# Optimization experiments

Measured on AMD Instinct MI355X. Metric: run time of the kernel, lower is better.

Reference implementation:

```python
import jax, jax.numpy as jnp
import numpy as np

N, E = 100000, 1600000          # nodes, edges
DIN, DH, DOUT = 128, 128, 64    # input_dim, hidden_dim, output_dim


def setup_inputs() -> dict:
    key = jax.random.key(0)
    k0, k1, k2, k3 = jax.random.split(key, 4)
    x = jax.random.normal(k0, (N, DIN), dtype=jnp.float32)
    edge_index = jax.random.randint(k1, (2, E), 0, N)
    # GCNConv params (glorot-ish weights, zero bias)
    W1 = jax.random.normal(k2, (DIN, DH), dtype=jnp.float32) / np.sqrt(DIN).astype(np.float32)
    b1 = jnp.zeros((DH,), jnp.float32)
    W2 = jax.random.normal(k3, (DH, DOUT), dtype=jnp.float32) / np.sqrt(DH).astype(np.float32)
    b2 = jnp.zeros((DOUT,), jnp.float32)
    return {"x": x, "edge_index": edge_index, "W1": W1, "b1": b1, "W2": W2, "b2": b2}


def _gcn_conv(h_in, W, b, src, dst, norm_e, self_norm, n):
    # PyG GCNConv: transform, then normalized sum-aggregation with self-loops.
    h = h_in @ W                                   # [N, dout]
    msg = h[src] * norm_e[:, None]                 # [E, dout] gather + edge scale
    agg = jax.ops.segment_sum(msg, dst, num_segments=n)
    agg = agg + h * self_norm[:, None]             # self-loop contribution (norm = 1/deg)
    return agg + b


def reference(x, edge_index, W1, b1, W2, b2):
    src, dst = edge_index[0], edge_index[1]
    n = x.shape[0]
    # degree including self-loop, computed on dst (PyG convention)
    deg = jax.ops.segment_sum(jnp.ones((src.shape[0],), x.dtype), dst, num_segments=n) + 1.0
    dinv = jax.lax.rsqrt(deg)
    norm_e = dinv[src] * dinv[dst]                 # per-edge D^-1/2 A D^-1/2
    self_norm = dinv * dinv
    h = _gcn_conv(x, W1, b1, src, dst, norm_e, self_norm, n)
    h = jax.nn.relu(h)                             # dropout is identity in eval mode
    out = _gcn_conv(h, W2, b2, src, dst, norm_e, self_norm, n)
    return out
```

## Files before the change

kernel.cpp:

```cpp
#include <hip/hip_runtime.h>

#define NN 100000
#define NE 1600000
#define NBUCK 1563
#define NBH 256
#define CHUNK 6250
#define NSEG 8
#define SEGC (NBH/NSEG)
#define NBXB 12500
#define NBG 1563
#define NBGG 782


typedef short bf16x8 __attribute__((ext_vector_type(8)));
typedef float f32x4  __attribute__((ext_vector_type(4)));
typedef float f32x2  __attribute__((ext_vector_type(2)));

__device__ __forceinline__ float b2f(unsigned short u) {
    return __uint_as_float(((unsigned int)u) << 16);
}
__device__ __forceinline__ unsigned short f2b(float f) {
    unsigned int x = __float_as_uint(f);
    x += 0x7FFFu + ((x >> 16) & 1u);
    return (unsigned short)(x >> 16);
}

__global__ __launch_bounds__(256) void k_pre(const float* __restrict__ x,
                                             unsigned short* __restrict__ xb,
                                             const int* __restrict__ dst,
                                             int* __restrict__ ghist,
                                             const float* __restrict__ W1,
                                             const float* __restrict__ W2,
                                             unsigned short* __restrict__ Wg1,
                                             unsigned short* __restrict__ Wg2) {
    int b = blockIdx.x;
    if (b < NBXB) {
        int id = b * 256 + threadIdx.x;
        float4 v = ((const float4*)x)[id];
        ushort4 o;
        o.x = f2b(v.x); o.y = f2b(v.y); o.z = f2b(v.z); o.w = f2b(v.w);
        ((ushort4*)xb)[id] = o;
        return;
    }
    if (b == NBXB + NBH) {
        for (int i = threadIdx.x; i < 16384; i += 256) {
            int j = i & 7, l = (i >> 3) & 63, ks = (i >> 9) & 3, ct = i >> 11;
            int k = ks * 32 + ((l >> 4) << 3) + j;
            int c = ct * 16 + (l & 15);
            Wg1[i] = f2b(W1[k * 128 + c]);
        }
        return;
    }
    if (b == NBXB + NBH + 1) {
        for (int i = threadIdx.x; i < 8192; i += 256) {
            int j = i & 7, l = (i >> 3) & 63, ks = (i >> 9) & 3, ct = i >> 11;
            int k = ks * 32 + ((l >> 4) << 3) + j;
            int c = ct * 16 + (l & 15);
            Wg2[i] = f2b(W2[k * 64 + c]);
        }
        return;
    }
    __shared__ int h[NBUCK];
    int tid = threadIdx.x;
    int i = b - NBXB;
    for (int k = tid; k < NBUCK; k += 256) h[k] = 0;
    __syncthreads();
    int e0 = i * CHUNK;
    for (int e = e0 + tid; e < e0 + CHUNK; e += 256) {
        unsigned d = (unsigned)dst[e];
        if (d < NN) atomicAdd(&h[d >> 6], 1);
    }
    __syncthreads();
    for (int k = tid; k < NBUCK; k += 256) ghist[i * NBUCK + k] = h[k];
}

__global__ __launch_bounds__(256) void k_scanB(const int* __restrict__ ghist,
                                               int* __restrict__ boffT,
                                               int* __restrict__ tot) {
    __shared__ int part[NSEG][32];
    int kk = threadIdx.x & 31, seg = threadIdx.x >> 5;
    int k = blockIdx.x * 32 + kk;
    bool ok = (k < NBUCK);
    int i0 = seg * SEGC;
    int S = 0;
    if (ok) {
#pragma unroll 8
        for (int i = i0; i < i0 + SEGC; ++i) S += ghist[i * NBUCK + k];
    }
    part[seg][kk] = S;
    __syncthreads();
    int pre = 0;
#pragma unroll
    for (int s2 = 0; s2 < NSEG; ++s2) pre += (s2 < seg) ? part[s2][kk] : 0;
    if (ok) {
        int run = pre;
#pragma unroll 8
        for (int i = i0; i < i0 + SEGC; ++i) {
            int c = ghist[i * NBUCK + k];
            boffT[i * NBUCK + k] = run;
            run += c;
        }
        if (seg == NSEG - 1) tot[k] = run;
    }
}

__global__ __launch_bounds__(256) void k_place(const int* __restrict__ src,
                                               const int* __restrict__ dst,
                                               const int* __restrict__ tot,
                                               const int* __restrict__ boffT,
                                               int* __restrict__ ebuf,
                                               int* __restrict__ bbase_out) {
    __shared__ int cur[NBUCK];
    __shared__ int s[256];
    const int tid = threadIdx.x, bid = blockIdx.x;
    const int i = ((bid & 7) * (NBH / 8)) + (bid >> 3);
    int k0 = tid * 7;
    int v[7]; int S = 0;
#pragma unroll
    for (int q = 0; q < 7; ++q) {
        int k = k0 + q;
        v[q] = (k < NBUCK) ? tot[k] : 0;
        S += v[q];
    }
    s[tid] = S;
    __syncthreads();
    for (int off = 1; off < 256; off <<= 1) {
        int t = (tid >= off) ? s[tid - off] : 0;
        __syncthreads();
        s[tid] += t;
        __syncthreads();
    }
    int run = s[tid] - S;
#pragma unroll
    for (int q = 0; q < 7; ++q) {
        int k = k0 + q;
        if (k < NBUCK) {
            cur[k] = run + boffT[i * NBUCK + k];
            if (bid == 0) bbase_out[k] = run;
            run += v[q];
        }
    }
    __syncthreads();
    int e0 = i * CHUNK;
    for (int e = e0 + tid; e < e0 + CHUNK; e += 256) {
        unsigned d = (unsigned)dst[e];
        if (d >= NN) continue;
        unsigned sv = (unsigned)src[e];
        if (sv >= NN) sv = 0;
        int pos = atomicAdd(&cur[d >> 6], 1);
        ebuf[pos] = (int)(sv | ((d & 63u) << 17));
    }
}

__global__ __launch_bounds__(256) void k_binC(const int* __restrict__ bbase,
                                              const int* __restrict__ tot,
                                              const int* __restrict__ ebuf,
                                              int* __restrict__ row_start,
                                              float* __restrict__ dinv,
                                              int* __restrict__ csr) {
    __shared__ int cnt[64], excl[64], cur[64];
    int b = blockIdx.x, tid = threadIdx.x;
    int n0 = b * 64;
    int base = bbase[b], end = base + tot[b];
    if (tid < 64) cnt[tid] = 0;
    __syncthreads();
    for (int i = base + tid; i < end; i += 256)
        atomicAdd(&cnt[((unsigned)ebuf[i]) >> 17], 1);
    __syncthreads();
    if (tid == 0) {
        int run = 0;
        for (int t = 0; t < 64; ++t) { excl[t] = run; run += cnt[t]; }
    }
    __syncthreads();
    if (tid < 64) {
        int node = n0 + tid;
        if (node < NN) {
            row_start[node] = base + excl[tid];
            dinv[node] = rsqrtf((float)cnt[tid] + 1.0f);
        }
        cur[tid] = base + excl[tid];
    }
    if (b == NBUCK - 1 && tid == 0) row_start[NN] = end;
    __syncthreads();
    for (int i = base + tid; i < end; i += 256) {
        unsigned rec = (unsigned)ebuf[i];
        int pos = atomicAdd(&cur[rec >> 17], 1);
        csr[pos] = (int)(rec & 0x1FFFFu);
    }
}

__global__ __launch_bounds__(256) void k_agg1(const unsigned short* __restrict__ xb,
                                              const float* __restrict__ dinv,
                                              const int* __restrict__ row_start,
                                              const int* __restrict__ csr,
                                              char* __restrict__ P) {
    int node = blockIdx.x * 4 + (threadIdx.x >> 6);
    int lane = threadIdx.x & 63;
    int sub  = lane >> 4;
    int dimb = lane & 15;
    const uint4* X4 = (const uint4*)xb;
    float dv = dinv[node];
    float sn4 = dv * dv * 0.25f;
    uint4 sv = X4[(size_t)node * 16 + dimb];
    f32x2 a0, a1, a2, a3;
    a0.x = __uint_as_float(sv.x << 16) * sn4;  a0.y = __uint_as_float(sv.x & 0xFFFF0000u) * sn4;
    a1.x = __uint_as_float(sv.y << 16) * sn4;  a1.y = __uint_as_float(sv.y & 0xFFFF0000u) * sn4;
    a2.x = __uint_as_float(sv.z << 16) * sn4;  a2.y = __uint_as_float(sv.z & 0xFFFF0000u) * sn4;
    a3.x = __uint_as_float(sv.w << 16) * sn4;  a3.y = __uint_as_float(sv.w & 0xFFFF0000u) * sn4;
    int base = row_start[node], end = row_start[node + 1];
    for (int c0 = base; c0 < end; c0 += 64) {
        int idx = c0 + lane;
        int cl = min(idx, end - 1);
        int s = csr[cl];
        float wv = (idx < end) ? dinv[s] * dv : 0.f;
        int ng = min(64, end - c0);
        for (int g = 0; g * 4 < ng; ++g) {
            int   sq = __shfl(s,  g * 4 + sub);
            float wq = __shfl(wv, g * 4 + sub);
            uint4 v = X4[(size_t)sq * 16 + dimb];
            f32x2 wv2; wv2.x = wq; wv2.y = wq;
            f32x2 xv;
            xv.x = __uint_as_float(v.x << 16); xv.y = __uint_as_float(v.x & 0xFFFF0000u);
            a0 = __builtin_elementwise_fma(xv, wv2, a0);
            xv.x = __uint_as_float(v.y << 16); xv.y = __uint_as_float(v.y & 0xFFFF0000u);
            a1 = __builtin_elementwise_fma(xv, wv2, a1);
            xv.x = __uint_as_float(v.z << 16); xv.y = __uint_as_float(v.z & 0xFFFF0000u);
            a2 = __builtin_elementwise_fma(xv, wv2, a2);
            xv.x = __uint_as_float(v.w << 16); xv.y = __uint_as_float(v.w & 0xFFFF0000u);
            a3 = __builtin_elementwise_fma(xv, wv2, a3);
        }
    }
#pragma unroll
    for (int mgap = 16; mgap < 64; mgap <<= 1) {
        a0.x += __shfl_xor(a0.x, mgap); a0.y += __shfl_xor(a0.y, mgap);
        a1.x += __shfl_xor(a1.x, mgap); a1.y += __shfl_xor(a1.y, mgap);
        a2.x += __shfl_xor(a2.x, mgap); a2.y += __shfl_xor(a2.y, mgap);
        a3.x += __shfl_xor(a3.x, mgap); a3.y += __shfl_xor(a3.y, mgap);
    }
    if (lane < 16) {
        uint4 o;
        o.x = (unsigned)f2b(a0.x) | ((unsigned)f2b(a0.y) << 16);
        o.y = (unsigned)f2b(a1.x) | ((unsigned)f2b(a1.y) << 16);
        o.z = (unsigned)f2b(a2.x) | ((unsigned)f2b(a2.y) << 16);
        o.w = (unsigned)f2b(a3.x) | ((unsigned)f2b(a3.y) << 16);
        ((uint4*)(P + (size_t)node * 256))[lane] = o;
    }
}

__global__ __launch_bounds__(256) void k_gemm12(const unsigned short* __restrict__ Wg1,
                                                const float* __restrict__ b1,
                                                const unsigned short* __restrict__ Wg2,
                                                char* __restrict__ P) {
    __shared__ __align__(16) short Cl[4][16][136];
    const int tid = threadIdx.x;
    const int w = tid >> 6, lane = tid & 63;
    const int quad = lane >> 4, l15 = lane & 15;

    float bias1[8];
#pragma unroll
    for (int ct = 0; ct < 8; ++ct) bias1[ct] = b1[ct * 16 + l15];

    for (int t = blockIdx.x; t < NBG; t += NBGG) {
        const int r0 = t * 64;
        const int m = r0 + w * 16 + l15;
        const bool mok = (m < NN);
        bf16x8 a[4];
#pragma unroll
        for (int ks = 0; ks < 4; ++ks) {
            if (mok) a[ks] = *(const bf16x8*)(P + (size_t)m * 256 + (ks * 32 + quad * 8) * 2);
            else     a[ks] = bf16x8{0,0,0,0,0,0,0,0};
        }
#pragma unroll
        for (int ct = 0; ct < 8; ++ct) {
            f32x4 c = {0.f, 0.f, 0.f, 0.f};
#pragma unroll
            for (int ks = 0; ks < 4; ++ks) {
                bf16x8 b = *(const bf16x8*)&Wg1[((ct * 4 + ks) * 64 + lane) * 8];
                c = __builtin_amdgcn_mfma_f32_16x16x32_bf16(a[ks], b, c, 0, 0, 0);
            }
#pragma unroll
            for (int r = 0; r < 4; ++r)
                Cl[w][quad * 4 + r][ct * 16 + l15] =
                    (short)f2b(fmaxf(c[r] + bias1[ct], 0.f));
        }
        __syncthreads();
        bf16x8 a2[4];
#pragma unroll
        for (int ks = 0; ks < 4; ++ks)
            a2[ks] = *(const bf16x8*)&Cl[w][l15][ks * 32 + quad * 8];
#pragma unroll
        for (int ct = 0; ct < 4; ++ct) {
            f32x4 c = {0.f, 0.f, 0.f, 0.f};
#pragma unroll
            for (int ks = 0; ks < 4; ++ks) {
                bf16x8 b = *(const bf16x8*)&Wg2[((ct * 4 + ks) * 64 + lane) * 8];
                c = __builtin_amdgcn_mfma_f32_16x16x32_bf16(a2[ks], b, c, 0, 0, 0);
            }
#pragma unroll
            for (int r = 0; r < 4; ++r) {
                int node = r0 + w * 16 + quad * 4 + r;
                if (node < NN)
                    *(unsigned short*)(P + (size_t)node * 256 + (ct * 16 + l15) * 2) =
                        f2b(c[r]);
            }
        }
        __syncthreads();
    }
}

__global__ __launch_bounds__(256) void k_agg2(const float* __restrict__ dinv,
                                              const int* __restrict__ row_start,
                                              const int* __restrict__ csr,
                                              const char* __restrict__ P,
                                              const float* __restrict__ b2,
                                              float* __restrict__ outp) {
    int node = blockIdx.x * 4 + (threadIdx.x >> 6);
    int lane = threadIdx.x & 63;
    int sub  = lane >> 3;
    int dimb = lane & 7;
    const uint4* P4 = (const uint4*)P;
    float dv = dinv[node];
    float sn8 = dv * dv * 0.125f;
    uint4 sv = P4[(size_t)node * 16 + dimb];
    f32x2 a0, a1, a2, a3;
    a0.x = __uint_as_float(sv.x << 16) * sn8;  a0.y = __uint_as_float(sv.x & 0xFFFF0000u) * sn8;
    a1.x = __uint_as_float(sv.y << 16) * sn8;  a1.y = __uint_as_float(sv.y & 0xFFFF0000u) * sn8;
    a2.x = __uint_as_float(sv.z << 16) * sn8;  a2.y = __uint_as_float(sv.z & 0xFFFF0000u) * sn8;
    a3.x = __uint_as_float(sv.w << 16) * sn8;  a3.y = __uint_as_float(sv.w & 0xFFFF0000u) * sn8;
    int base = row_start[node], end = row_start[node + 1];
    if (end > base) {
        for (int c0 = base; c0 < end; c0 += 64) {
            int idx = c0 + lane;
            int cl = min(idx, end - 1);
            int s = csr[cl];
            float wv = (idx < end) ? dinv[s] * dv : 0.f;
            int ng = min(64, end - c0);
            for (int g = 0; g * 8 < ng; ++g) {
                int   sq = __shfl(s,  g * 8 + sub);
                float wq = __shfl(wv, g * 8 + sub);
                uint4 v = P4[(size_t)sq * 16 + dimb];
                f32x2 wv2; wv2.x = wq; wv2.y = wq;
                f32x2 xv;
                xv.x = __uint_as_float(v.x << 16); xv.y = __uint_as_float(v.x & 0xFFFF0000u);
                a0 = __builtin_elementwise_fma(xv, wv2, a0);
                xv.x = __uint_as_float(v.y << 16); xv.y = __uint_as_float(v.y & 0xFFFF0000u);
                a1 = __builtin_elementwise_fma(xv, wv2, a1);
                xv.x = __uint_as_float(v.z << 16); xv.y = __uint_as_float(v.z & 0xFFFF0000u);
                a2 = __builtin_elementwise_fma(xv, wv2, a2);
                xv.x = __uint_as_float(v.w << 16); xv.y = __uint_as_float(v.w & 0xFFFF0000u);
                a3 = __builtin_elementwise_fma(xv, wv2, a3);
            }
        }
    }
#pragma unroll
    for (int mgap = 8; mgap < 64; mgap <<= 1) {
        a0.x += __shfl_xor(a0.x, mgap); a0.y += __shfl_xor(a0.y, mgap);
        a1.x += __shfl_xor(a1.x, mgap); a1.y += __shfl_xor(a1.y, mgap);
        a2.x += __shfl_xor(a2.x, mgap); a2.y += __shfl_xor(a2.y, mgap);
        a3.x += __shfl_xor(a3.x, mgap); a3.y += __shfl_xor(a3.y, mgap);
    }
    if (lane < 8) {
        float4 ba = ((const float4*)b2)[lane * 2];
        float4 bb = ((const float4*)b2)[lane * 2 + 1];
        float4 o0, o1;
        o0.x = a0.x + ba.x; o0.y = a0.y + ba.y; o0.z = a1.x + ba.z; o0.w = a1.y + ba.w;
        o1.x = a2.x + bb.x; o1.y = a2.y + bb.y; o1.z = a3.x + bb.z; o1.w = a3.y + bb.w;
        ((float4*)outp)[(size_t)node * 16 + lane * 2]     = o0;
        ((float4*)outp)[(size_t)node * 16 + lane * 2 + 1] = o1;
    }
}

extern "C" void kernel_launch(void* const* d_in, const int* in_sizes, int n_in,
                              void* d_out, int out_size, void* d_ws, size_t ws_size,
                              hipStream_t stream) {
    const float* x  = (const float*)d_in[0];
    const int*   ei = (const int*)d_in[1];
    const float* W1 = (const float*)d_in[2];
    const float* b1 = (const float*)d_in[3];
    const float* W2 = (const float*)d_in[4];
    const float* b2 = (const float*)d_in[5];
    float* out = (float*)d_out;
    const int* src = ei;
    const int* dst = ei + NE;

    char* ws = (char*)d_ws;
    unsigned short* xb        = (unsigned short*)(ws + 0);
    char*           P         = ws + 25600000;
    int*            ghist     = (int*)(ws + 25600000);
    int*            boffT     = (int*)(ws + 27200512);
    int*            tot       = (int*)(ws + 28801024);
    int*            bbase     = (int*)(ws + 28807276);
    int*            row_start = (int*)(ws + 51200000);
    float*          dinv      = (float*)(ws + 51600004);
    int*            csr       = (int*)(ws + 52000004);
    int*            ebuf      = (int*)(ws + 58400004);
    unsigned short* Wg1       = (unsigned short*)(ws + 64800004);
    unsigned short* Wg2       = (unsigned short*)(ws + 64832772);

    k_pre  <<<NBXB + NBH + 2, 256, 0, stream>>>(x, xb, dst, ghist, W1, W2, Wg1, Wg2);
    k_scanB<<<(NBUCK + 31) / 32, 256, 0, stream>>>(ghist, boffT, tot);
    k_place<<<NBH, 256, 0, stream>>>(src, dst, tot, boffT, ebuf, bbase);
    k_binC <<<NBUCK, 256, 0, stream>>>(bbase, tot, ebuf, row_start, dinv, csr);

    k_agg1  <<<NN / 4, 256, 0, stream>>>(xb, dinv, row_start, csr, P);
    k_gemm12<<<NBGG, 256, 0, stream>>>(Wg1, b1, Wg2, P);
    k_agg2  <<<NN / 4, 256, 0, stream>>>(dinv, row_start, csr, P, b2, out);
}
```

Baseline: 280.9 us.

## Fuse layer-1 aggregation with both GEMMs and compact the T2 layout

Merges the first aggregation kernel into the two-GEMM kernel. Each block aggregates 64 nodes into shared memory and feeds them straight into the MFMA layers, so the aggregated bf16 intermediate no longer round-trips through global memory. The second-layer transform is written to a compact 64-wide T2 buffer instead of a 256-byte-stride slot, which halves the per-row footprint read by the second aggregation. In exchange there is one fewer launch but much less parallelism for the gather: each wave now walks 16 nodes in sequence across only 1563 blocks, and the extra LDS use may lower occupancy.

```diff
diff --git a/kernel.cpp b/kernel.cpp
--- a/kernel.cpp
+++ b/kernel.cpp
@@ -9,7 +9,6 @@
 #define SEGC (NBH/NSEG)
 #define NBXB 12500
 #define NBG 1563
-#define NBGG 782
 
 
 typedef short bf16x8 __attribute__((ext_vector_type(8)));
@@ -189,139 +188,141 @@
     }
 }
 
-__global__ __launch_bounds__(256) void k_agg1(const unsigned short* __restrict__ xb,
+__global__ __launch_bounds__(256) void k_ag1g(const unsigned short* __restrict__ xb,
                                               const float* __restrict__ dinv,
                                               const int* __restrict__ row_start,
                                               const int* __restrict__ csr,
-                                              char* __restrict__ P) {
-    int node = blockIdx.x * 4 + (threadIdx.x >> 6);
-    int lane = threadIdx.x & 63;
-    int sub  = lane >> 4;
-    int dimb = lane & 15;
-    const uint4* X4 = (const uint4*)xb;
-    float dv = dinv[node];
-    float sn4 = dv * dv * 0.25f;
-    uint4 sv = X4[(size_t)node * 16 + dimb];
-    f32x2 a0, a1, a2, a3;
-    a0.x = __uint_as_float(sv.x << 16) * sn4;  a0.y = __uint_as_float(sv.x & 0xFFFF0000u) * sn4;
-    a1.x = __uint_as_float(sv.y << 16) * sn4;  a1.y = __uint_as_float(sv.y & 0xFFFF0000u) * sn4;
-    a2.x = __uint_as_float(sv.z << 16) * sn4;  a2.y = __uint_as_float(sv.z & 0xFFFF0000u) * sn4;
-    a3.x = __uint_as_float(sv.w << 16) * sn4;  a3.y = __uint_as_float(sv.w & 0xFFFF0000u) * sn4;
-    int base = row_start[node], end = row_start[node + 1];
-    for (int c0 = base; c0 < end; c0 += 64) {
-        int idx = c0 + lane;
-        int cl = min(idx, end - 1);
-        int s = csr[cl];
-        float wv = (idx < end) ? dinv[s] * dv : 0.f;
-        int ng = min(64, end - c0);
-        for (int g = 0; g * 4 < ng; ++g) {
-            int   sq = __shfl(s,  g * 4 + sub);
-            float wq = __shfl(wv, g * 4 + sub);
-            uint4 v = X4[(size_t)sq * 16 + dimb];
-            f32x2 wv2; wv2.x = wq; wv2.y = wq;
-            f32x2 xv;
-            xv.x = __uint_as_float(v.x << 16); xv.y = __uint_as_float(v.x & 0xFFFF0000u);
-            a0 = __builtin_elementwise_fma(xv, wv2, a0);
-            xv.x = __uint_as_float(v.y << 16); xv.y = __uint_as_float(v.y & 0xFFFF0000u);
-            a1 = __builtin_elementwise_fma(xv, wv2, a1);
-            xv.x = __uint_as_float(v.z << 16); xv.y = __uint_as_float(v.z & 0xFFFF0000u);
-            a2 = __builtin_elementwise_fma(xv, wv2, a2);
-            xv.x = __uint_as_float(v.w << 16); xv.y = __uint_as_float(v.w & 0xFFFF0000u);
-            a3 = __builtin_elementwise_fma(xv, wv2, a3);
-        }
-    }
-#pragma unroll
-    for (int mgap = 16; mgap < 64; mgap <<= 1) {
-        a0.x += __shfl_xor(a0.x, mgap); a0.y += __shfl_xor(a0.y, mgap);
-        a1.x += __shfl_xor(a1.x, mgap); a1.y += __shfl_xor(a1.y, mgap);
-        a2.x += __shfl_xor(a2.x, mgap); a2.y += __shfl_xor(a2.y, mgap);
-        a3.x += __shfl_xor(a3.x, mgap); a3.y += __shfl_xor(a3.y, mgap);
-    }
-    if (lane < 16) {
-        uint4 o;
-        o.x = (unsigned)f2b(a0.x) | ((unsigned)f2b(a0.y) << 16);
-        o.y = (unsigned)f2b(a1.x) | ((unsigned)f2b(a1.y) << 16);
-        o.z = (unsigned)f2b(a2.x) | ((unsigned)f2b(a2.y) << 16);
-        o.w = (unsigned)f2b(a3.x) | ((unsigned)f2b(a3.y) << 16);
-        ((uint4*)(P + (size_t)node * 256))[lane] = o;
-    }
-}
-
-__global__ __launch_bounds__(256) void k_gemm12(const unsigned short* __restrict__ Wg1,
-                                                const float* __restrict__ b1,
-                                                const unsigned short* __restrict__ Wg2,
-                                                char* __restrict__ P) {
+                                              const unsigned short* __restrict__ Wg1,
+                                              const float* __restrict__ b1,
+                                              const unsigned short* __restrict__ Wg2,
+                                              unsigned short* __restrict__ T2) {
+    __shared__ __align__(16) short Pl[64][136];
     __shared__ __align__(16) short Cl[4][16][136];
     const int tid = threadIdx.x;
     const int w = tid >> 6, lane = tid & 63;
     const int quad = lane >> 4, l15 = lane & 15;
+    const int sub  = lane >> 4;
+    const int dimb = lane & 15;
+    const uint4* X4 = (const uint4*)xb;
+    const int r0 = blockIdx.x * 64;
 
     float bias1[8];
 #pragma unroll
     for (int ct = 0; ct < 8; ++ct) bias1[ct] = b1[ct * 16 + l15];
 
-    for (int t = blockIdx.x; t < NBG; t += NBGG) {
-        const int r0 = t * 64;
-        const int m = r0 + w * 16 + l15;
-        const bool mok = (m < NN);
-        bf16x8 a[4];
+    for (int nl = 0; nl < 16; ++nl) {
+        int n_loc = w * 16 + nl;
+        int node = r0 + n_loc;
+        if (node < NN) {
+            float dv = dinv[node];
+            float sn4 = dv * dv * 0.25f;
+            uint4 sv = X4[(size_t)node * 16 + dimb];
+            f32x2 a0, a1, a2, a3;
+            a0.x = __uint_as_float(sv.x << 16) * sn4;  a0.y = __uint_as_float(sv.x & 0xFFFF0000u) * sn4;
+            a1.x = __uint_as_float(sv.y << 16) * sn4;  a1.y = __uint_as_float(sv.y & 0xFFFF0000u) * sn4;
+            a2.x = __uint_as_float(sv.z << 16) * sn4;  a2.y = __uint_as_float(sv.z & 0xFFFF0000u) * sn4;
+            a3.x = __uint_as_float(sv.w << 16) * sn4;  a3.y = __uint_as_float(sv.w & 0xFFFF0000u) * sn4;
+            int base = row_start[node], end = row_start[node + 1];
+            for (int c0 = base; c0 < end; c0 += 64) {
+                int idx = c0 + lane;
+                int cl = min(idx, end - 1);
+                int s = csr[cl];
+                float wv = (idx < end) ? dinv[s] * dv : 0.f;
+                int ng = min(64, end - c0);
+                for (int g = 0; g * 4 < ng; ++g) {
+                    int   sq = __shfl(s,  g * 4 + sub);
+                    float wq = __shfl(wv, g * 4 + sub);
+                    uint4 v = X4[(size_t)sq * 16 + dimb];
+                    f32x2 wv2; wv2.x = wq; wv2.y = wq;
+                    f32x2 xv;
+                    xv.x = __uint_as_float(v.x << 16); xv.y = __uint_as_float(v.x & 0xFFFF0000u);
+                    a0 = __builtin_elementwise_fma(xv, wv2, a0);
+                    xv.x = __uint_as_float(v.y << 16); xv.y = __uint_as_float(v.y & 0xFFFF0000u);
+                    a1 = __builtin_elementwise_fma(xv, wv2, a1);
+                    xv.x = __uint_as_float(v.z << 16); xv.y = __uint_as_float(v.z & 0xFFFF0000u);
+                    a2 = __builtin_elementwise_fma(xv, wv2, a2);
+                    xv.x = __uint_as_float(v.w << 16); xv.y = __uint_as_float(v.w & 0xFFFF0000u);
+                    a3 = __builtin_elementwise_fma(xv, wv2, a3);
+                }
+            }
+#pragma unroll
+            for (int mgap = 16; mgap < 64; mgap <<= 1) {
+                a0.x += __shfl_xor(a0.x, mgap); a0.y += __shfl_xor(a0.y, mgap);
+                a1.x += __shfl_xor(a1.x, mgap); a1.y += __shfl_xor(a1.y, mgap);
+                a2.x += __shfl_xor(a2.x, mgap); a2.y += __shfl_xor(a2.y, mgap);
+                a3.x += __shfl_xor(a3.x, mgap); a3.y += __shfl_xor(a3.y, mgap);
+            }
+            if (lane < 16) {
+                uint4 o;
+                o.x = (unsigned)f2b(a0.x) | ((unsigned)f2b(a0.y) << 16);
+                o.y = (unsigned)f2b(a1.x) | ((unsigned)f2b(a1.y) << 16);
+                o.z = (unsigned)f2b(a2.x) | ((unsigned)f2b(a2.y) << 16);
+                o.w = (unsigned)f2b(a3.x) | ((unsigned)f2b(a3.y) << 16);
+                *(uint4*)&Pl[n_loc][lane * 8] = o;
+            }
+        } else {
+            if (lane < 16) {
+                uint4 z; z.x = 0; z.y = 0; z.z = 0; z.w = 0;
+                *(uint4*)&Pl[n_loc][lane * 8] = z;
+            }
+        }
+    }
+    __syncthreads();
+
+    bf16x8 a[4];
+#pragma unroll
+    for (int ks = 0; ks < 4; ++ks)
+        a[ks] = *(const bf16x8*)&Pl[w * 16 + l15][ks * 32 + quad * 8];
+#pragma unroll
+    for (int ct = 0; ct < 8; ++ct) {
+        f32x4 c = {0.f, 0.f, 0.f, 0.f};
 #pragma unroll
         for (int ks = 0; ks < 4; ++ks) {
-            if (mok) a[ks] = *(const bf16x8*)(P + (size_t)m * 256 + (ks * 32 + quad * 8) * 2);
-            else     a[ks] = bf16x8{0,0,0,0,0,0,0,0};
-        }
-#pragma unroll
-        for (int ct = 0; ct < 8; ++ct) {
-            f32x4 c = {0.f, 0.f, 0.f, 0.f};
-#pragma unroll
-            for (int ks = 0; ks < 4; ++ks) {
-                bf16x8 b = *(const bf16x8*)&Wg1[((ct * 4 + ks) * 64 + lane) * 8];
-                c = __builtin_amdgcn_mfma_f32_16x16x32_bf16(a[ks], b, c, 0, 0, 0);
-            }
-#pragma unroll
-            for (int r = 0; r < 4; ++r)
-                Cl[w][quad * 4 + r][ct * 16 + l15] =
-                    (short)f2b(fmaxf(c[r] + bias1[ct], 0.f));
-        }
-        __syncthreads();
-        bf16x8 a2[4];
-#pragma unroll
-        for (int ks = 0; ks < 4; ++ks)
-            a2[ks] = *(const bf16x8*)&Cl[w][l15][ks * 32 + quad * 8];
-#pragma unroll
-        for (int ct = 0; ct < 4; ++ct) {
-            f32x4 c = {0.f, 0.f, 0.f, 0.f};
-#pragma unroll
-            for (int ks = 0; ks < 4; ++ks) {
-                bf16x8 b = *(const bf16x8*)&Wg2[((ct * 4 + ks) * 64 + lane) * 8];
-                c = __builtin_amdgcn_mfma_f32_16x16x32_bf16(a2[ks], b, c, 0, 0, 0);
-            }
-#pragma unroll
-            for (int r = 0; r < 4; ++r) {
-                int node = r0 + w * 16 + quad * 4 + r;
-                if (node < NN)
-                    *(unsigned short*)(P + (size_t)node * 256 + (ct * 16 + l15) * 2) =
-                        f2b(c[r]);
-            }
-        }
-        __syncthreads();
+            bf16x8 b = *(const bf16x8*)&Wg1[((ct * 4 + ks) * 64 + lane) * 8];
+            c = __builtin_amdgcn_mfma_f32_16x16x32_bf16(a[ks], b, c, 0, 0, 0);
+        }
+#pragma unroll
+        for (int r = 0; r < 4; ++r)
+            Cl[w][quad * 4 + r][ct * 16 + l15] =
+                (short)f2b(fmaxf(c[r] + bias1[ct], 0.f));
+    }
+    __syncthreads();
+
+    bf16x8 a2[4];
+#pragma unroll
+    for (int ks = 0; ks < 4; ++ks)
+        a2[ks] = *(const bf16x8*)&Cl[w][l15][ks * 32 + quad * 8];
+#pragma unroll
+    for (int ct = 0; ct < 4; ++ct) {
+        f32x4 c = {0.f, 0.f, 0.f, 0.f};
+#pragma unroll
+        for (int ks = 0; ks < 4; ++ks) {
+            bf16x8 b = *(const bf16x8*)&Wg2[((ct * 4 + ks) * 64 + lane) * 8];
+            c = __builtin_amdgcn_mfma_f32_16x16x32_bf16(a2[ks], b, c, 0, 0, 0);
+        }
+#pragma unroll
+        for (int r = 0; r < 4; ++r) {
+            int node = r0 + w * 16 + quad * 4 + r;
+            if (node < NN)
+                T2[(size_t)node * 64 + ct * 16 + l15] = f2b(c[r]);
+        }
     }
 }
 
 __global__ __launch_bounds__(256) void k_agg2(const float* __restrict__ dinv,
                                               const int* __restrict__ row_start,
                                               const int* __restrict__ csr,
-                                              const char* __restrict__ P,
+                                              const unsigned short* __restrict__ T2,
                                               const float* __restrict__ b2,
                                               float* __restrict__ outp) {
     int node = blockIdx.x * 4 + (threadIdx.x >> 6);
     int lane = threadIdx.x & 63;
     int sub  = lane >> 3;
     int dimb = lane & 7;
-    const uint4* P4 = (const uint4*)P;
+    const uint4* T4 = (const uint4*)T2;
     float dv = dinv[node];
     float sn8 = dv * dv * 0.125f;
-    uint4 sv = P4[(size_t)node * 16 + dimb];
+    uint4 sv = T4[(size_t)node * 8 + dimb];
     f32x2 a0, a1, a2, a3;
     a0.x = __uint_as_float(sv.x << 16) * sn8;  a0.y = __uint_as_float(sv.x & 0xFFFF0000u) * sn8;
     a1.x = __uint_as_float(sv.y << 16) * sn8;  a1.y = __uint_as_float(sv.y & 0xFFFF0000u) * sn8;
@@ -338,7 +339,7 @@
             for (int g = 0; g * 8 < ng; ++g) {
                 int   sq = __shfl(s,  g * 8 + sub);
                 float wq = __shfl(wv, g * 8 + sub);
-                uint4 v = P4[(size_t)sq * 16 + dimb];
+                uint4 v = T4[(size_t)sq * 8 + dimb];
                 f32x2 wv2; wv2.x = wq; wv2.y = wq;
                 f32x2 xv;
                 xv.x = __uint_as_float(v.x << 16); xv.y = __uint_as_float(v.x & 0xFFFF0000u);
@@ -385,7 +386,7 @@
 
     char* ws = (char*)d_ws;
     unsigned short* xb        = (unsigned short*)(ws + 0);
-    char*           P         = ws + 25600000;
+    unsigned short* T2        = (unsigned short*)(ws + 25600000);
     int*            ghist     = (int*)(ws + 25600000);
     int*            boffT     = (int*)(ws + 27200512);
     int*            tot       = (int*)(ws + 28801024);
@@ -402,7 +403,6 @@
     k_place<<<NBH, 256, 0, stream>>>(src, dst, tot, boffT, ebuf, bbase);
     k_binC <<<NBUCK, 256, 0, stream>>>(bbase, tot, ebuf, row_start, dinv, csr);
 
-    k_agg1  <<<NN / 4, 256, 0, stream>>>(xb, dinv, row_start, csr, P);
-    k_gemm12<<<NBGG, 256, 0, stream>>>(Wg1, b1, Wg2, P);
-    k_agg2  <<<NN / 4, 256, 0, stream>>>(dinv, row_start, csr, P, b2, out);
-}
+    k_ag1g <<<NBG, 256, 0, stream>>>(xb, dinv, row_start, csr, Wg1, b1, Wg2, T2);
+    k_agg2 <<<NN / 4, 256, 0, stream>>>(dinv, row_start, csr, T2, b2, out);
+}
```

After: 315.6 us. 12.4% more time.
